# Kernel tuning notes

Hardware: AMD Instinct MI355X
Metric: run time of the kernel (lower is better)

## Reference

```python
import jax, jax.numpy as jnp
import numpy as np

B, T, D = 64, 2048, 512
UNITS = 512


def setup_inputs() -> dict:
    key = jax.random.key(0)
    ks = jax.random.split(key, 8)
    s = 1.0 / np.sqrt(D)
    return {
        "decoder_hidden": jax.random.normal(ks[0], (B, D), dtype=jnp.float32),
        "encoder_output": jax.random.normal(ks[1], (B, T, D), dtype=jnp.float32),
        "W1": jax.random.normal(ks[2], (D, UNITS), dtype=jnp.float32) * s,
        "b1": jnp.zeros((UNITS,), dtype=jnp.float32),
        "W2": jax.random.normal(ks[3], (D, UNITS), dtype=jnp.float32) * s,
        "b2": jnp.zeros((UNITS,), dtype=jnp.float32),
        "V": jax.random.normal(ks[4], (UNITS, 1), dtype=jnp.float32) * (1.0 / np.sqrt(UNITS)),
        "bV": jnp.zeros((1,), dtype=jnp.float32),
    }


def reference(decoder_hidden, encoder_output, W1, b1, W2, b2, V, bV):
    # query projection: [B, 1, U]
    q = (decoder_hidden @ W1 + b1)[:, None, :]
    # key projection: [B, T, U]
    k = jnp.einsum('btd,du->btu', encoder_output, W2) + b2
    score = jnp.tanh(q + k)                       # [B, T, U]
    logits = score @ V + bV                       # [B, T, 1]
    attention_weights = jax.nn.softmax(logits, axis=1)  # [B, T, 1]
    context_vector = jnp.sum(attention_weights * encoder_output, axis=1)  # [B, D]
    return context_vector, attention_weights
```

## Files before the change

### kernel.cpp

```cpp
#include <hip/hip_runtime.h>
#include <stdint.h>

constexpr int NB = 64;
constexpr int NT = 2048;
constexpr int ND = 512;
constexpr int NU = 512;

typedef float f32x4 __attribute__((ext_vector_type(4)));
typedef float f32x16 __attribute__((ext_vector_type(16)));
typedef short bf16x8 __attribute__((ext_vector_type(8)));

__device__ __forceinline__ unsigned short f2bf(float x) {
  union { float f; unsigned int u; } v; v.f = x;
  unsigned int r = v.u + 0x7FFFu + ((v.u >> 16) & 1u);
  return (unsigned short)(r >> 16);
}

__device__ __forceinline__ float fast_tanh(float x) {
  return 1.0f - 2.0f / (__expf(2.0f * x) + 1.0f);
}

__global__ __launch_bounds__(512) void qproj_kernel(
    const float* __restrict__ dh, const float* __restrict__ W1,
    const float* __restrict__ b1, const float* __restrict__ b2,
    float* __restrict__ q) {
  int b = blockIdx.x;
  int u = threadIdx.x;
  const float* dr = dh + b * ND;
  float a0 = 0.f, a1 = 0.f, a2 = 0.f, a3 = 0.f;
  for (int k = 0; k < ND; k += 4) {
    a0 = fmaf(dr[k + 0], W1[(size_t)(k + 0) * NU + u], a0);
    a1 = fmaf(dr[k + 1], W1[(size_t)(k + 1) * NU + u], a1);
    a2 = fmaf(dr[k + 2], W1[(size_t)(k + 2) * NU + u], a2);
    a3 = fmaf(dr[k + 3], W1[(size_t)(k + 3) * NU + u], a3);
  }
  q[b * NU + u] = b1[u] + b2[u] + ((a0 + a1) + (a2 + a3));
}

__global__ __launch_bounds__(256) void packW2_kernel(
    const float* __restrict__ W2, unsigned short* __restrict__ w2p) {
  int tid = blockIdx.x * 256 + threadIdx.x;
  int lane = tid & 63;
  int ntg = (tid >> 6) & 15;
  int ks = tid >> 10;
  int col = ntg * 32 + (lane & 31);
  int k0 = ks * 16 + ((lane >> 5) << 3);
  const float* src = W2 + (size_t)k0 * NU + col;
  ushort4 lo, hi;
  lo.x = f2bf(src[0 * NU]); lo.y = f2bf(src[1 * NU]);
  lo.z = f2bf(src[2 * NU]); lo.w = f2bf(src[3 * NU]);
  hi.x = f2bf(src[4 * NU]); hi.y = f2bf(src[5 * NU]);
  hi.z = f2bf(src[6 * NU]); hi.w = f2bf(src[7 * NU]);
  ushort4* dst = (ushort4*)(w2p + (size_t)tid * 8);
  dst[0] = lo; dst[1] = hi;
}

__global__ __launch_bounds__(512, 4) void logits_kernel(
    const float* __restrict__ enc, const unsigned short* __restrict__ w2p,
    const float* __restrict__ q, const float* __restrict__ Vw,
    float* __restrict__ logits) {
  __shared__ unsigned short encA[64 * 512];
  __shared__ float red[8][64];

  const int tid = threadIdx.x;
  const int wave = tid >> 6;
  const int lane = tid & 63;
  const int wg = blockIdx.x;
  const int b = wg >> 5;
  const int tch = wg & 31;
  const char* w2pc = (const char*)w2p;

  const int rot = wave * 4;
  const int bsub = ((2 * wave) * 64 + lane) * 16;

  int voffB = rot * 16384 + bsub;
  bf16x8 b0a = *(const bf16x8*)(w2pc + voffB);
  bf16x8 b0b = *(const bf16x8*)(w2pc + voffB + 1024);
  voffB = (voffB + 16384) & 0x7FFFF;
  bf16x8 b1a = *(const bf16x8*)(w2pc + voffB);
  bf16x8 b1b = *(const bf16x8*)(w2pc + voffB + 1024);
  voffB = (voffB + 16384) & 0x7FFFF;

  const float4* encBase = (const float4*)(enc + ((size_t)b * NT + (size_t)tch * 64) * ND);
#pragma unroll
  for (int i = 0; i < 8; ++i) {
    int idx8 = i * 512 + tid;
    int row = idx8 >> 6;
    int c8 = idx8 & 63;
    float4 v0 = encBase[idx8 * 2];
    float4 v1 = encBase[idx8 * 2 + 1];
    unsigned int p0, p1, p2, p3;
    asm("v_cvt_pk_bf16_f32 %0, %1, %2" : "=v"(p0) : "v"(v0.x), "v"(v0.y));
    asm("v_cvt_pk_bf16_f32 %0, %1, %2" : "=v"(p1) : "v"(v0.z), "v"(v0.w));
    asm("v_cvt_pk_bf16_f32 %0, %1, %2" : "=v"(p2) : "v"(v1.x), "v"(v1.y));
    asm("v_cvt_pk_bf16_f32 %0, %1, %2" : "=v"(p3) : "v"(v1.z), "v"(v1.w));
    uint4 pk; pk.x = p0; pk.y = p1; pk.z = p2; pk.w = p3;
    int byteoff = row * 1024 + ((c8 * 16) ^ ((row & 7) << 4));
    *(uint4*)((char*)encA + byteoff) = pk;
  }

  f32x16 acc00 = {}, acc01 = {}, acc10 = {}, acc11 = {};

  const int arow0 = (lane & 31) * 1024;
  const int arow1 = arow0 + 32 * 1024;
  const int aswz = ((lane & 31) & 7) << 4;
  const int kfix = (lane >> 5) << 4;
  int kaBase = rot * 32 + kfix;
  const char* encAc = (const char*)encA;

  __syncthreads();

#pragma unroll
  for (int i = 0; i < 32; i += 2) {
    int ka = kaBase ^ aswz;
    kaBase = (kaBase + 32) & 1023;
    bf16x8 a0 = *(const bf16x8*)(encAc + arow0 + ka);
    bf16x8 a1 = *(const bf16x8*)(encAc + arow1 + ka);
    bf16x8 n0a = *(const bf16x8*)(w2pc + voffB);
    bf16x8 n0b = *(const bf16x8*)(w2pc + voffB + 1024);
    voffB = (voffB + 16384) & 0x7FFFF;
    __builtin_amdgcn_s_setprio(1);
    acc00 = __builtin_amdgcn_mfma_f32_32x32x16_bf16(a0, b0a, acc00, 0, 0, 0);
    acc01 = __builtin_amdgcn_mfma_f32_32x32x16_bf16(a0, b0b, acc01, 0, 0, 0);
    acc10 = __builtin_amdgcn_mfma_f32_32x32x16_bf16(a1, b0a, acc10, 0, 0, 0);
    acc11 = __builtin_amdgcn_mfma_f32_32x32x16_bf16(a1, b0b, acc11, 0, 0, 0);
    __builtin_amdgcn_s_setprio(0);
    b0a = n0a; b0b = n0b;

    int kb = kaBase ^ aswz;
    kaBase = (kaBase + 32) & 1023;
    bf16x8 a2 = *(const bf16x8*)(encAc + arow0 + kb);
    bf16x8 a3 = *(const bf16x8*)(encAc + arow1 + kb);
    bf16x8 n1a = *(const bf16x8*)(w2pc + voffB);
    bf16x8 n1b = *(const bf16x8*)(w2pc + voffB + 1024);
    voffB = (voffB + 16384) & 0x7FFFF;
    __builtin_amdgcn_s_setprio(1);
    acc00 = __builtin_amdgcn_mfma_f32_32x32x16_bf16(a2, b1a, acc00, 0, 0, 0);
    acc01 = __builtin_amdgcn_mfma_f32_32x32x16_bf16(a2, b1b, acc01, 0, 0, 0);
    acc10 = __builtin_amdgcn_mfma_f32_32x32x16_bf16(a3, b1a, acc10, 0, 0, 0);
    acc11 = __builtin_amdgcn_mfma_f32_32x32x16_bf16(a3, b1b, acc11, 0, 0, 0);
    __builtin_amdgcn_s_setprio(0);
    b1a = n1a; b1b = n1b;
  }

  const int col = lane & 31;
  const float qv0 = q[b * NU + wave * 64 + col];
  const float qv1 = q[b * NU + wave * 64 + 32 + col];
  const float Vv0 = Vw[wave * 64 + col];
  const float Vv1 = Vw[wave * 64 + 32 + col];
  const int hi4 = (lane >> 5) << 2;

#pragma unroll
  for (int amt = 0; amt < 2; ++amt) {
#pragma unroll
    for (int reg = 0; reg < 16; ++reg) {
      float c0 = amt ? acc10[reg] : acc00[reg];
      float c1 = amt ? acc11[reg] : acc01[reg];
      float s = fast_tanh(c0 + qv0) * Vv0 + fast_tanh(c1 + qv1) * Vv1;
      s += __shfl_xor(s, 1);
      s += __shfl_xor(s, 2);
      s += __shfl_xor(s, 4);
      s += __shfl_xor(s, 8);
      s += __shfl_xor(s, 16);
      if (col == 0) {
        int row = (reg & 3) + ((reg >> 2) << 3) + hi4;
        red[wave][amt * 32 + row] = s;
      }
    }
  }
  __syncthreads();
  if (tid < 64) {
    float t = 0.f;
#pragma unroll
    for (int w = 0; w < 8; ++w) t += red[w][tid];
    logits[(size_t)b * NT + (size_t)tch * 64 + tid] = t;
  }
}

__global__ __launch_bounds__(512) void softmax_kernel(float* __restrict__ wts) {
  int b = blockIdx.x;
  int tid = threadIdx.x;
  float4* base = (float4*)(wts + (size_t)b * NT);
  float4 v = base[tid];
  float m = fmaxf(fmaxf(v.x, v.y), fmaxf(v.z, v.w));
#pragma unroll
  for (int d = 1; d < 64; d <<= 1) m = fmaxf(m, __shfl_xor(m, d));
  __shared__ float sm[8];
  __shared__ float ss[8];
  int w = tid >> 6;
  if ((tid & 63) == 0) sm[w] = m;
  __syncthreads();
  float M = sm[0];
#pragma unroll
  for (int i = 1; i < 8; ++i) M = fmaxf(M, sm[i]);
  float e0 = __expf(v.x - M), e1 = __expf(v.y - M), e2 = __expf(v.z - M), e3 = __expf(v.w - M);
  float s = e0 + e1 + e2 + e3;
#pragma unroll
  for (int d = 1; d < 64; d <<= 1) s += __shfl_xor(s, d);
  if ((tid & 63) == 0) ss[w] = s;
  __syncthreads();
  float S = 0.f;
#pragma unroll
  for (int i = 0; i < 8; ++i) S += ss[i];
  float inv = 1.0f / S;
  base[tid] = (float4){e0 * inv, e1 * inv, e2 * inv, e3 * inv};
}

__global__ __launch_bounds__(512) void ctx_partial_kernel(
    const float* __restrict__ enc, const float* __restrict__ wts,
    float* __restrict__ partials) {
  int bx = blockIdx.x;
  int b = bx >> 4;
  int slice = bx & 15;
  int tid = threadIdx.x;
  const float* e = enc + ((size_t)b * NT + (size_t)slice * 128) * ND + tid;
  const float* wp = wts + (size_t)b * NT + slice * 128;
  float acc = 0.0f;
#pragma unroll 4
  for (int tt = 0; tt < 128; ++tt) {
    acc = fmaf(wp[tt], e[(size_t)tt * ND], acc);
  }
  partials[(size_t)bx * ND + tid] = acc;
}

__global__ __launch_bounds__(512) void ctx_combine_kernel(
    const float* __restrict__ partials, float* __restrict__ ctx) {
  int b = blockIdx.x;
  int tid = threadIdx.x;
  float s = 0.0f;
#pragma unroll
  for (int i = 0; i < 16; ++i) s += partials[((size_t)b * 16 + i) * ND + tid];
  ctx[(size_t)b * ND + tid] = s;
}

extern "C" void kernel_launch(void* const* d_in, const int* in_sizes, int n_in,
                              void* d_out, int out_size, void* d_ws, size_t ws_size,
                              hipStream_t stream) {
  const float* dh  = (const float*)d_in[0];
  const float* enc = (const float*)d_in[1];
  const float* W1  = (const float*)d_in[2];
  const float* b1  = (const float*)d_in[3];
  const float* W2  = (const float*)d_in[4];
  const float* b2  = (const float*)d_in[5];
  const float* Vw  = (const float*)d_in[6];

  float* q            = (float*)d_ws;
  unsigned short* w2p = (unsigned short*)((char*)d_ws + 131072);
  float* partials     = (float*)((char*)d_ws + 655360);

  float* ctx = (float*)d_out;
  float* wts = (float*)d_out + NB * ND;

  qproj_kernel<<<NB, 512, 0, stream>>>(dh, W1, b1, b2, q);
  packW2_kernel<<<128, 256, 0, stream>>>(W2, w2p);
  logits_kernel<<<NB * (NT / 64), 512, 0, stream>>>(enc, w2p, q, Vw, wts);
  softmax_kernel<<<NB, 512, 0, stream>>>(wts);
  ctx_partial_kernel<<<NB * 16, 512, 0, stream>>>(enc, wts, partials);
  ctx_combine_kernel<<<NB, 512, 0, stream>>>(partials, ctx);
}
```

Before: 177.9 us.

## Make logits kernel persistent with double-buffered LDS prefetch of encoder tiles

```diff
diff --git a/kernel.cpp b/kernel.cpp
--- a/kernel.cpp
+++ b/kernel.cpp
@@ -55,127 +55,170 @@
   dst[0] = lo; dst[1] = hi;
 }
 
-__global__ __launch_bounds__(512, 4) void logits_kernel(
+#define PHASE(BA, BB)                                                              \
+  {                                                                                \
+    int ka = kaBase ^ aswz; kaBase = (kaBase + 32) & 1023;                         \
+    bf16x8 a0 = *(const bf16x8*)(ec + arow0 + ka);                                 \
+    bf16x8 a1 = *(const bf16x8*)(ec + arow1 + ka);                                 \
+    __builtin_amdgcn_s_setprio(1);                                                 \
+    acc00 = __builtin_amdgcn_mfma_f32_32x32x16_bf16(a0, BA, acc00, 0, 0, 0);       \
+    acc01 = __builtin_amdgcn_mfma_f32_32x32x16_bf16(a0, BB, acc01, 0, 0, 0);       \
+    acc10 = __builtin_amdgcn_mfma_f32_32x32x16_bf16(a1, BA, acc10, 0, 0, 0);       \
+    acc11 = __builtin_amdgcn_mfma_f32_32x32x16_bf16(a1, BB, acc11, 0, 0, 0);       \
+    __builtin_amdgcn_s_setprio(0);                                                 \
+    BA = *(const bf16x8*)(w2pc + voffB);                                           \
+    BB = *(const bf16x8*)(w2pc + voffB + 1024);                                    \
+    voffB = (voffB + 16384) & 0x7FFFF;                                             \
+  }
+
+__global__ __launch_bounds__(512, 2) void logits_kernel(
     const float* __restrict__ enc, const unsigned short* __restrict__ w2p,
     const float* __restrict__ q, const float* __restrict__ Vw,
     float* __restrict__ logits) {
-  __shared__ unsigned short encA[64 * 512];
+  __shared__ unsigned short encA[2][64 * 512];
   __shared__ float red[8][64];
 
   const int tid = threadIdx.x;
   const int wave = tid >> 6;
   const int lane = tid & 63;
-  const int wg = blockIdx.x;
-  const int b = wg >> 5;
-  const int tch = wg & 31;
+  const int p = blockIdx.x;
   const char* w2pc = (const char*)w2p;
+  const float4* encf4 = (const float4*)enc;
 
   const int rot = wave * 4;
   const int bsub = ((2 * wave) * 64 + lane) * 16;
-
   int voffB = rot * 16384 + bsub;
+
   bf16x8 b0a = *(const bf16x8*)(w2pc + voffB);
   bf16x8 b0b = *(const bf16x8*)(w2pc + voffB + 1024);
   voffB = (voffB + 16384) & 0x7FFFF;
   bf16x8 b1a = *(const bf16x8*)(w2pc + voffB);
   bf16x8 b1b = *(const bf16x8*)(w2pc + voffB + 1024);
   voffB = (voffB + 16384) & 0x7FFFF;
-
-  const float4* encBase = (const float4*)(enc + ((size_t)b * NT + (size_t)tch * 64) * ND);
-#pragma unroll
-  for (int i = 0; i < 8; ++i) {
-    int idx8 = i * 512 + tid;
-    int row = idx8 >> 6;
-    int c8 = idx8 & 63;
-    float4 v0 = encBase[idx8 * 2];
-    float4 v1 = encBase[idx8 * 2 + 1];
-    unsigned int p0, p1, p2, p3;
-    asm("v_cvt_pk_bf16_f32 %0, %1, %2" : "=v"(p0) : "v"(v0.x), "v"(v0.y));
-    asm("v_cvt_pk_bf16_f32 %0, %1, %2" : "=v"(p1) : "v"(v0.z), "v"(v0.w));
-    asm("v_cvt_pk_bf16_f32 %0, %1, %2" : "=v"(p2) : "v"(v1.x), "v"(v1.y));
-    asm("v_cvt_pk_bf16_f32 %0, %1, %2" : "=v"(p3) : "v"(v1.z), "v"(v1.w));
-    uint4 pk; pk.x = p0; pk.y = p1; pk.z = p2; pk.w = p3;
-    int byteoff = row * 1024 + ((c8 * 16) ^ ((row & 7) << 4));
-    *(uint4*)((char*)encA + byteoff) = pk;
-  }
-
-  f32x16 acc00 = {}, acc01 = {}, acc10 = {}, acc11 = {};
+  bf16x8 b2a = *(const bf16x8*)(w2pc + voffB);
+  bf16x8 b2b = *(const bf16x8*)(w2pc + voffB + 1024);
+  voffB = (voffB + 16384) & 0x7FFFF;
+  bf16x8 b3a = *(const bf16x8*)(w2pc + voffB);
+  bf16x8 b3b = *(const bf16x8*)(w2pc + voffB + 1024);
+  voffB = (voffB + 16384) & 0x7FFFF;
 
   const int arow0 = (lane & 31) * 1024;
   const int arow1 = arow0 + 32 * 1024;
-  const int aswz = ((lane & 31) & 7) << 4;
+  const int aswz = (lane & 31) << 4;
   const int kfix = (lane >> 5) << 4;
-  int kaBase = rot * 32 + kfix;
-  const char* encAc = (const char*)encA;
-
-  __syncthreads();
-
-#pragma unroll
-  for (int i = 0; i < 32; i += 2) {
-    int ka = kaBase ^ aswz;
-    kaBase = (kaBase + 32) & 1023;
-    bf16x8 a0 = *(const bf16x8*)(encAc + arow0 + ka);
-    bf16x8 a1 = *(const bf16x8*)(encAc + arow1 + ka);
-    bf16x8 n0a = *(const bf16x8*)(w2pc + voffB);
-    bf16x8 n0b = *(const bf16x8*)(w2pc + voffB + 1024);
-    voffB = (voffB + 16384) & 0x7FFFF;
-    __builtin_amdgcn_s_setprio(1);
-    acc00 = __builtin_amdgcn_mfma_f32_32x32x16_bf16(a0, b0a, acc00, 0, 0, 0);
-    acc01 = __builtin_amdgcn_mfma_f32_32x32x16_bf16(a0, b0b, acc01, 0, 0, 0);
-    acc10 = __builtin_amdgcn_mfma_f32_32x32x16_bf16(a1, b0a, acc10, 0, 0, 0);
-    acc11 = __builtin_amdgcn_mfma_f32_32x32x16_bf16(a1, b0b, acc11, 0, 0, 0);
-    __builtin_amdgcn_s_setprio(0);
-    b0a = n0a; b0b = n0b;
-
-    int kb = kaBase ^ aswz;
-    kaBase = (kaBase + 32) & 1023;
-    bf16x8 a2 = *(const bf16x8*)(encAc + arow0 + kb);
-    bf16x8 a3 = *(const bf16x8*)(encAc + arow1 + kb);
-    bf16x8 n1a = *(const bf16x8*)(w2pc + voffB);
-    bf16x8 n1b = *(const bf16x8*)(w2pc + voffB + 1024);
-    voffB = (voffB + 16384) & 0x7FFFF;
-    __builtin_amdgcn_s_setprio(1);
-    acc00 = __builtin_amdgcn_mfma_f32_32x32x16_bf16(a2, b1a, acc00, 0, 0, 0);
-    acc01 = __builtin_amdgcn_mfma_f32_32x32x16_bf16(a2, b1b, acc01, 0, 0, 0);
-    acc10 = __builtin_amdgcn_mfma_f32_32x32x16_bf16(a3, b1a, acc10, 0, 0, 0);
-    acc11 = __builtin_amdgcn_mfma_f32_32x32x16_bf16(a3, b1b, acc11, 0, 0, 0);
-    __builtin_amdgcn_s_setprio(0);
-    b1a = n1a; b1b = n1b;
-  }
 
   const int col = lane & 31;
-  const float qv0 = q[b * NU + wave * 64 + col];
-  const float qv1 = q[b * NU + wave * 64 + 32 + col];
   const float Vv0 = Vw[wave * 64 + col];
   const float Vv1 = Vw[wave * 64 + 32 + col];
   const int hi4 = (lane >> 5) << 2;
 
-#pragma unroll
-  for (int amt = 0; amt < 2; ++amt) {
-#pragma unroll
-    for (int reg = 0; reg < 16; ++reg) {
-      float c0 = amt ? acc10[reg] : acc00[reg];
-      float c1 = amt ? acc11[reg] : acc01[reg];
-      float s = fast_tanh(c0 + qv0) * Vv0 + fast_tanh(c1 + qv1) * Vv1;
-      s += __shfl_xor(s, 1);
-      s += __shfl_xor(s, 2);
-      s += __shfl_xor(s, 4);
-      s += __shfl_xor(s, 8);
-      s += __shfl_xor(s, 16);
-      if (col == 0) {
-        int row = (reg & 3) + ((reg >> 2) << 3) + hi4;
-        red[wave][amt * 32 + row] = s;
+  {
+    const float4* eb = encf4 + (size_t)p * 8192;
+    char* dst = (char*)encA[0];
+#pragma unroll
+    for (int j = 0; j < 8; ++j) {
+      int idx8 = j * 512 + tid;
+      int row = idx8 >> 6;
+      int c8 = idx8 & 63;
+      float4 v0 = eb[idx8 * 2];
+      float4 v1 = eb[idx8 * 2 + 1];
+      unsigned int p0, p1, p2, p3;
+      asm("v_cvt_pk_bf16_f32 %0, %1, %2" : "=v"(p0) : "v"(v0.x), "v"(v0.y));
+      asm("v_cvt_pk_bf16_f32 %0, %1, %2" : "=v"(p1) : "v"(v0.z), "v"(v0.w));
+      asm("v_cvt_pk_bf16_f32 %0, %1, %2" : "=v"(p2) : "v"(v1.x), "v"(v1.y));
+      asm("v_cvt_pk_bf16_f32 %0, %1, %2" : "=v"(p3) : "v"(v1.z), "v"(v1.w));
+      uint4 pk; pk.x = p0; pk.y = p1; pk.z = p2; pk.w = p3;
+      *(uint4*)(dst + row * 1024 + ((c8 * 16) ^ ((row & 31) << 4))) = pk;
+    }
+  }
+  __syncthreads();
+
+  for (int t = 0; t < 8; ++t) {
+    const int T = p + t * 256;
+    const char* ec = (const char*)encA[t & 1];
+    char* en = (char*)encA[(t & 1) ^ 1];
+
+    float4 f0, f1, f2, f3, f4, f5, f6, f7, f8, f9, f10, f11, f12, f13, f14, f15;
+    if (t < 7) {
+      const float4* eb = encf4 + (size_t)(T + 256) * 8192;
+      f0  = eb[0 * 1024 + tid * 2];  f1  = eb[0 * 1024 + tid * 2 + 1];
+      f2  = eb[1 * 1024 + tid * 2];  f3  = eb[1 * 1024 + tid * 2 + 1];
+      f4  = eb[2 * 1024 + tid * 2];  f5  = eb[2 * 1024 + tid * 2 + 1];
+      f6  = eb[3 * 1024 + tid * 2];  f7  = eb[3 * 1024 + tid * 2 + 1];
+      f8  = eb[4 * 1024 + tid * 2];  f9  = eb[4 * 1024 + tid * 2 + 1];
+      f10 = eb[5 * 1024 + tid * 2];  f11 = eb[5 * 1024 + tid * 2 + 1];
+      f12 = eb[6 * 1024 + tid * 2];  f13 = eb[6 * 1024 + tid * 2 + 1];
+      f14 = eb[7 * 1024 + tid * 2];  f15 = eb[7 * 1024 + tid * 2 + 1];
+    }
+    const int qb = (T >> 5) * NU + wave * 64 + col;
+    const float qv0 = q[qb];
+    const float qv1 = q[qb + 32];
+
+    f32x16 acc00 = {}, acc01 = {}, acc10 = {}, acc11 = {};
+    int kaBase = rot * 32 + kfix;
+
+    for (int i = 0; i < 16; i += 4) {
+      PHASE(b0a, b0b)
+      PHASE(b1a, b1b)
+      PHASE(b2a, b2b)
+      PHASE(b3a, b3b)
+    }
+
+    if (t < 7) {
+#define STW(J, VA, VB)                                                             \
+      {                                                                            \
+        int idx8 = (J) * 512 + tid;                                                \
+        int row = idx8 >> 6;                                                       \
+        int c8 = idx8 & 63;                                                        \
+        unsigned int p0, p1, p2, p3;                                               \
+        asm("v_cvt_pk_bf16_f32 %0, %1, %2" : "=v"(p0) : "v"(VA.x), "v"(VA.y));     \
+        asm("v_cvt_pk_bf16_f32 %0, %1, %2" : "=v"(p1) : "v"(VA.z), "v"(VA.w));     \
+        asm("v_cvt_pk_bf16_f32 %0, %1, %2" : "=v"(p2) : "v"(VB.x), "v"(VB.y));     \
+        asm("v_cvt_pk_bf16_f32 %0, %1, %2" : "=v"(p3) : "v"(VB.z), "v"(VB.w));     \
+        uint4 pk; pk.x = p0; pk.y = p1; pk.z = p2; pk.w = p3;                      \
+        *(uint4*)(en + row * 1024 + ((c8 * 16) ^ ((row & 31) << 4))) = pk;         \
       }
-    }
-  }
-  __syncthreads();
-  if (tid < 64) {
-    float t = 0.f;
-#pragma unroll
-    for (int w = 0; w < 8; ++w) t += red[w][tid];
-    logits[(size_t)b * NT + (size_t)tch * 64 + tid] = t;
-  }
-}
+      STW(0, f0, f1)   STW(1, f2, f3)   STW(2, f4, f5)   STW(3, f6, f7)
+      STW(4, f8, f9)   STW(5, f10, f11) STW(6, f12, f13) STW(7, f14, f15)
+#undef STW
+    }
+
+    for (int i = 0; i < 16; i += 4) {
+      PHASE(b0a, b0b)
+      PHASE(b1a, b1b)
+      PHASE(b2a, b2b)
+      PHASE(b3a, b3b)
+    }
+
+#pragma unroll
+    for (int amt = 0; amt < 2; ++amt) {
+#pragma unroll
+      for (int reg = 0; reg < 16; ++reg) {
+        float c0 = amt ? acc10[reg] : acc00[reg];
+        float c1 = amt ? acc11[reg] : acc01[reg];
+        float s = fast_tanh(c0 + qv0) * Vv0 + fast_tanh(c1 + qv1) * Vv1;
+        s += __shfl_xor(s, 1);
+        s += __shfl_xor(s, 2);
+        s += __shfl_xor(s, 4);
+        s += __shfl_xor(s, 8);
+        s += __shfl_xor(s, 16);
+        if (col == 0) {
+          int row = (reg & 3) + ((reg >> 2) << 3) + hi4;
+          red[wave][amt * 32 + row] = s;
+        }
+      }
+    }
+    __syncthreads();
+    if (tid < 64) {
+      float s = 0.f;
+#pragma unroll
+      for (int w = 0; w < 8; ++w) s += red[w][tid];
+      logits[(size_t)T * 64 + tid] = s;
+    }
+    __syncthreads();
+  }
+}
+#undef PHASE
 
 __global__ __launch_bounds__(512) void softmax_kernel(float* __restrict__ wts) {
   int b = blockIdx.x;
@@ -253,7 +296,7 @@
 
   qproj_kernel<<<NB, 512, 0, stream>>>(dh, W1, b1, b2, q);
   packW2_kernel<<<128, 256, 0, stream>>>(W2, w2p);
-  logits_kernel<<<NB * (NT / 64), 512, 0, stream>>>(enc, w2p, q, Vw, wts);
+  logits_kernel<<<256, 512, 0, stream>>>(enc, w2p, q, Vw, wts);
   softmax_kernel<<<NB, 512, 0, stream>>>(wts);
   ctx_partial_kernel<<<NB * 16, 512, 0, stream>>>(enc, wts, partials);
   ctx_combine_kernel<<<NB, 512, 0, stream>>>(partials, ctx);
```

Measured after the change: 394.7 us. 122% more time.
